# Optimization experiments

Hardware: AMD Instinct MI355X
Metric: run time of the kernel (lower is better)

The kernel has to match this reference:

```python
import jax, jax.numpy as jnp
import numpy as np

EPS = 1e-7


def setup_inputs() -> dict:
    key = jax.random.key(0)
    k1, k2, k3 = jax.random.split(key, 3)
    B, Nt, Nv, D = 64, 128, 256, 512
    text_feats = jax.random.normal(k1, (B, Nt, D), dtype=jnp.float32)
    visual_feats = jax.random.normal(k2, (B, Nv, D), dtype=jnp.float32)
    attention_mask = jax.random.randint(k3, (B, Nt), 0, 2, dtype=jnp.int32)
    return {"text_feats": text_feats, "visual_feats": visual_feats,
            "attention_mask": attention_mask}


def _l2norm(x):
    return x / jnp.clip(jnp.linalg.norm(x, axis=-1, keepdims=True), 1e-12)


def reference(text_feats, visual_feats, attention_mask):
    # Normalize token features (F.normalize along D)
    t = _l2norm(text_feats)            # (B, Nt, D)
    v = _l2norm(visual_feats)          # (B, Nv, D)
    # All-pairs token similarities: (B, B, Nt, Nv)
    token_sims = jnp.einsum('itd,jvd->ijtv', t, v)
    # Max over visual tokens -> (B, B, Nt)
    max_sims = jnp.max(token_sims, axis=3)
    # Masked mean over text tokens -> (B, B)
    mask = attention_mask.astype(jnp.float32)[:, None, :]   # (B, 1, Nt) broadcasts over pairs
    masked_sum = jnp.sum(max_sims * mask, axis=2)            # (B, B)
    valid = jnp.clip(jnp.sum(mask, axis=2), EPS)             # (B, 1)
    clip_sims = masked_sum / valid                           # (B, B)
    # Symmetric InfoNCE on the diagonal
    B = clip_sims.shape[0]
    diag = jnp.arange(B)
    losses_t2v = -jax.nn.log_softmax(clip_sims, axis=1)[diag, diag]
    losses_v2t = -jax.nn.log_softmax(clip_sims.T, axis=1)[diag, diag]
    contrastive_loss = jnp.mean(losses_t2v + losses_v2t) / 2.0
    # Regularization: keep negative token sims near zero
    neg_sims = jnp.clip(token_sims, -20.0, 0.0)
    reg_loss = 0.15 * jnp.mean(neg_sims ** 2)
    return contrastive_loss + reg_loss
```

## Files before the change

### kernel.cpp

```cpp
#include <hip/hip_runtime.h>
#include <hip/hip_bf16.h>

#define BB 64
#define NT 128
#define NV 256
#define DD 512
#define BKB 128
#define EPSF 1e-7f

typedef __attribute__((ext_vector_type(8))) int i32x8;
typedef __attribute__((ext_vector_type(4))) int i32x4;
typedef __attribute__((ext_vector_type(4))) float f32x4;

__device__ __forceinline__ void glds16(const uchar* g, uchar* l) {
    __builtin_amdgcn_global_load_lds(
        (const __attribute__((address_space(1))) unsigned int*)g,
        (__attribute__((address_space(3))) unsigned int*)l, 16, 0, 0);
}

__global__ __launch_bounds__(256) void k_normalize(
    const float* __restrict__ tf, const float* __restrict__ vf,
    uchar* __restrict__ tn, uchar* __restrict__ vn,
    float* __restrict__ reg_sum) {
    if (blockIdx.x == 0 && threadIdx.x == 0) *reg_sum = 0.0f;
    const int w = threadIdx.x >> 6, l = threadIdx.x & 63;
    const int row = blockIdx.x * 4 + w;
    const float* src;
    uchar* dst;
    if (row < BB * NT) {
        src = tf + (size_t)row * DD;
        dst = tn + (size_t)row * DD;
    } else {
        int r = row - BB * NT;
        src = vf + (size_t)r * DD;
        dst = vn + (size_t)r * DD;
    }
    float4 x0 = ((const float4*)src)[l * 2];
    float4 x1 = ((const float4*)src)[l * 2 + 1];
    float ss = x0.x * x0.x + x0.y * x0.y + x0.z * x0.z + x0.w * x0.w
             + x1.x * x1.x + x1.y * x1.y + x1.z * x1.z + x1.w * x1.w;
    #pragma unroll
    for (int off = 32; off; off >>= 1) ss += __shfl_xor(ss, off, 64);
    float scale = 1.0f / fmaxf(sqrtf(ss), 1e-12f);
    int p0 = __builtin_amdgcn_cvt_pk_fp8_f32(x0.x * scale, x0.y * scale, 0, 0);
    p0 = __builtin_amdgcn_cvt_pk_fp8_f32(x0.z * scale, x0.w * scale, p0, 1);
    int p1 = __builtin_amdgcn_cvt_pk_fp8_f32(x1.x * scale, x1.y * scale, 0, 0);
    p1 = __builtin_amdgcn_cvt_pk_fp8_f32(x1.z * scale, x1.w * scale, p1, 1);
    ((uint2*)dst)[l] = make_uint2((unsigned)p0, (unsigned)p1);
}

__global__ __launch_bounds__(512, 2) void k_gemm(
    const uchar* __restrict__ tn, const uchar* __restrict__ vn,
    const int* __restrict__ mask,
    float* __restrict__ clip_sims, float* __restrict__ reg_sum) {
    __shared__ uchar sT[NT * BKB];
    __shared__ uchar sV[NV * BKB];
    __shared__ float maxbuf[NT][4];
    __shared__ float redw[8];
    __shared__ float c0[2], c1[2];

    const int i = blockIdx.x, j = blockIdx.y;
    const int tid = threadIdx.x;
    const int l = tid & 63, w = tid >> 6;
    const int wr = w >> 2, wc = w & 3;
    const int m15 = l & 15, q = l >> 4;

    const uchar* tbase = tn + (size_t)i * NT * DD;
    const uchar* vbase = vn + (size_t)j * NV * DD;

    int t_off[2], v_off[4];
    #pragma unroll
    for (int s = 0; s < 2; ++s) {
        int f = s * 512 + tid;
        int r = f >> 3, p = f & 7, g = (p - r) & 7;
        t_off[s] = r * DD + g * 16;
    }
    #pragma unroll
    for (int s = 0; s < 4; ++s) {
        int f = s * 512 + tid;
        int r = f >> 3, p = f & 7, g = (p - r) & 7;
        v_off[s] = r * DD + g * 16;
    }

    int a_b0[4], a_b1[4], b_b0[4], b_b1[4];
    #pragma unroll
    for (int rt = 0; rt < 4; ++rt) {
        int row = wr * 64 + rt * 16 + m15;
        a_b0[rt] = row * BKB + (((2 * q + row) & 7) * 16);
        a_b1[rt] = row * BKB + (((2 * q + 1 + row) & 7) * 16);
    }
    #pragma unroll
    for (int ct = 0; ct < 4; ++ct) {
        int row = wc * 64 + ct * 16 + m15;
        b_b0[ct] = row * BKB + (((2 * q + row) & 7) * 16);
        b_b1[ct] = row * BKB + (((2 * q + 1 + row) & 7) * 16);
    }

    f32x4 acc[4][4];
    #pragma unroll
    for (int rt = 0; rt < 4; ++rt)
        #pragma unroll
        for (int ct = 0; ct < 4; ++ct) acc[rt][ct] = (f32x4){0.f, 0.f, 0.f, 0.f};

    for (int kk = 0; kk < DD; kk += BKB) {
        #pragma unroll
        for (int s = 0; s < 2; ++s)
            glds16(tbase + t_off[s] + kk, sT + (s * 512 + tid) * 16);
        #pragma unroll
        for (int s = 0; s < 4; ++s)
            glds16(vbase + v_off[s] + kk, sV + (s * 512 + tid) * 16);
        __syncthreads();

        i32x8 a[4];
        #pragma unroll
        for (int rt = 0; rt < 4; ++rt) {
            i32x4 lo = *(const i32x4*)(sT + a_b0[rt]);
            i32x4 hi = *(const i32x4*)(sT + a_b1[rt]);
            a[rt] = (i32x8){lo.x, lo.y, lo.z, lo.w, hi.x, hi.y, hi.z, hi.w};
        }
        #pragma unroll
        for (int ct = 0; ct < 4; ++ct) {
            i32x4 lo = *(const i32x4*)(sV + b_b0[ct]);
            i32x4 hi = *(const i32x4*)(sV + b_b1[ct]);
            i32x8 b = (i32x8){lo.x, lo.y, lo.z, lo.w, hi.x, hi.y, hi.z, hi.w};
            #pragma unroll
            for (int rt = 0; rt < 4; ++rt)
                acc[rt][ct] = __builtin_amdgcn_mfma_scale_f32_16x16x128_f8f6f4(
                    a[rt], b, acc[rt][ct],
                    0 , 0 ,
                    0, 127 , 0, 127 );
        }
        __syncthreads();
    }

    float rp = 0.0f;
    #pragma unroll
    for (int rt = 0; rt < 4; ++rt)
        #pragma unroll
        for (int ct = 0; ct < 4; ++ct)
            #pragma unroll
            for (int r = 0; r < 4; ++r) {
                float m = fminf(acc[rt][ct][r], 0.0f);
                rp = fmaf(m, m, rp);
            }

    #pragma unroll
    for (int rt = 0; rt < 4; ++rt)
        #pragma unroll
        for (int r = 0; r < 4; ++r) {
            float m = acc[rt][0][r];
            #pragma unroll
            for (int ct = 1; ct < 4; ++ct) m = fmaxf(m, acc[rt][ct][r]);
            #pragma unroll
            for (int msk = 1; msk < 16; msk <<= 1)
                m = fmaxf(m, __shfl_xor(m, msk, 64));
            if (m15 == 0)
                maxbuf[wr * 64 + rt * 16 + q * 4 + r][wc] = m;
        }

    #pragma unroll
    for (int off = 32; off; off >>= 1) rp += __shfl_down(rp, off, 64);
    if (l == 0) redw[w] = rp;
    __syncthreads();

    if (tid < NT) {
        float rm = fmaxf(fmaxf(maxbuf[tid][0], maxbuf[tid][1]),
                         fmaxf(maxbuf[tid][2], maxbuf[tid][3]));
        float mf = (float)mask[i * NT + tid];
        float v = rm * mf;
        #pragma unroll
        for (int off = 32; off; off >>= 1) {
            v += __shfl_down(v, off, 64);
            mf += __shfl_down(mf, off, 64);
        }
        if (l == 0) { c0[w] = v; c1[w] = mf; }
    }
    __syncthreads();
    if (tid == 0) {
        clip_sims[i * BB + j] = (c0[0] + c0[1]) / fmaxf(c1[0] + c1[1], EPSF);
        float s = 0.0f;
        #pragma unroll
        for (int x = 0; x < 8; ++x) s += redw[x];
        atomicAdd(reg_sum, s);
    }
}

__global__ __launch_bounds__(256) void k_loss(
    const float* __restrict__ clip_sims, const float* __restrict__ reg_sum,
    float* __restrict__ out) {
    __shared__ float sc[BB][BB + 1];
    __shared__ float lrow[BB], lcol[BB];
    int tid = threadIdx.x;
    for (int idx = tid; idx < BB * BB; idx += 256)
        sc[idx / BB][idx % BB] = clip_sims[idx];
    __syncthreads();
    if (tid < BB) {
        int i = tid;
        float m = sc[i][0];
        #pragma unroll
        for (int j = 1; j < BB; ++j) m = fmaxf(m, sc[i][j]);
        float s = 0.0f;
        #pragma unroll
        for (int j = 0; j < BB; ++j) s += expf(sc[i][j] - m);
        lrow[i] = m + logf(s) - sc[i][i];
    } else if (tid < 2 * BB) {
        int i = tid - BB;
        float m = sc[0][i];
        #pragma unroll
        for (int j = 1; j < BB; ++j) m = fmaxf(m, sc[j][i]);
        float s = 0.0f;
        #pragma unroll
        for (int j = 0; j < BB; ++j) s += expf(sc[j][i] - m);
        lcol[i] = m + logf(s) - sc[i][i];
    }
    __syncthreads();
    if (tid == 0) {
        float tot = 0.0f;
        for (int i = 0; i < BB; ++i) tot += lrow[i] + lcol[i];
        float contrastive = tot / (2.0f * BB);
        double denom = (double)BB * BB * NT * NV;
        float reg = 0.15f * (float)((double)reg_sum[0] / denom);
        out[0] = contrastive + reg;
    }
}

extern "C" void kernel_launch(void* const* d_in, const int* in_sizes, int n_in,
                              void* d_out, int out_size, void* d_ws, size_t ws_size,
                              hipStream_t stream) {
    const float* tf = (const float*)d_in[0];
    const float* vf = (const float*)d_in[1];
    const int* mask = (const int*)d_in[2];
    float* out = (float*)d_out;

    char* ws = (char*)d_ws;
    size_t tn_bytes = (size_t)BB * NT * DD;
    size_t vn_bytes = (size_t)BB * NV * DD;
    size_t cs_bytes = (size_t)BB * BB * sizeof(float);

    uchar* tn = (uchar*)ws;
    uchar* vn = (uchar*)(ws + tn_bytes);
    float* clip_sims = (float*)(ws + tn_bytes + vn_bytes);
    float* reg_sum = (float*)(ws + tn_bytes + vn_bytes + cs_bytes);

    k_normalize<<<(BB * NT + BB * NV) / 4, 256, 0, stream>>>(tf, vf, tn, vn, reg_sum);
    k_gemm<<<dim3(BB, BB), 512, 0, stream>>>(tn, vn, mask, clip_sims, reg_sum);
    k_loss<<<1, 256, 0, stream>>>(clip_sims, reg_sum, out);
}
```

Baseline: 250.0 us.

## Enlarge GEMM tile to two text samples, double-buffer LDS, swizzle block order

Each GEMM block now handles two text samples (256 rows) against one visual sample, so every B tile loaded into LDS is reused across twice as many rows. The K loop is fully unrolled and double-buffered, so the next K slice is prefetched into the alternate LDS buffer while MFMAs run on the current one. A 1D grid with a block-index swizzle groups blocks to improve L2 locality. In exchange the accumulators double to 128 floats per thread and LDS use grows to about 128KB, which may lower occupancy and cause register spills.

After: 419.5 us. +67.8%, slower.

```diff
diff --git a/kernel.cpp b/kernel.cpp
--- a/kernel.cpp
+++ b/kernel.cpp
@@ -6,6 +6,8 @@
 #define NV 256
 #define DD 512
 #define BKB 128
+#define BM 256
+#define BN 256
 #define EPSF 1e-7f
 
 typedef __attribute__((ext_vector_type(8))) int i32x8;
@@ -53,39 +55,37 @@
     const uchar* __restrict__ tn, const uchar* __restrict__ vn,
     const int* __restrict__ mask,
     float* __restrict__ clip_sims, float* __restrict__ reg_sum) {
-    __shared__ uchar sT[NT * BKB];
-    __shared__ uchar sV[NV * BKB];
-    __shared__ float maxbuf[NT][4];
+    __shared__ uchar sT[2][BM * BKB];
+    __shared__ uchar sV[2][BN * BKB];
+    __shared__ float maxbuf[BM][4];
     __shared__ float redw[8];
-    __shared__ float c0[2], c1[2];
-
-    const int i = blockIdx.x, j = blockIdx.y;
+    __shared__ float c0[4], c1[4];
+
+    const int bid = blockIdx.x;
+    const int swz = (bid & 7) * 256 + (bid >> 3);
+    const int bx = swz & 31;
+    const int by = swz >> 5;
+
     const int tid = threadIdx.x;
     const int l = tid & 63, w = tid >> 6;
     const int wr = w >> 2, wc = w & 3;
     const int m15 = l & 15, q = l >> 4;
 
-    const uchar* tbase = tn + (size_t)i * NT * DD;
-    const uchar* vbase = vn + (size_t)j * NV * DD;
-
-    int t_off[2], v_off[4];
-    #pragma unroll
-    for (int s = 0; s < 2; ++s) {
-        int f = s * 512 + tid;
-        int r = f >> 3, p = f & 7, g = (p - r) & 7;
-        t_off[s] = r * DD + g * 16;
-    }
+    const uchar* tbase = tn + (size_t)bx * BM * DD;
+    const uchar* vbase = vn + (size_t)by * NV * DD;
+
+    int soff[4];
     #pragma unroll
     for (int s = 0; s < 4; ++s) {
         int f = s * 512 + tid;
         int r = f >> 3, p = f & 7, g = (p - r) & 7;
-        v_off[s] = r * DD + g * 16;
-    }
-
-    int a_b0[4], a_b1[4], b_b0[4], b_b1[4];
-    #pragma unroll
-    for (int rt = 0; rt < 4; ++rt) {
-        int row = wr * 64 + rt * 16 + m15;
+        soff[s] = r * DD + g * 16;
+    }
+
+    int a_b0[8], a_b1[8], b_b0[4], b_b1[4];
+    #pragma unroll
+    for (int rt = 0; rt < 8; ++rt) {
+        int row = wr * 128 + rt * 16 + m15;
         a_b0[rt] = row * BKB + (((2 * q + row) & 7) * 16);
         a_b1[rt] = row * BKB + (((2 * q + 1 + row) & 7) * 16);
     }
@@ -96,46 +96,57 @@
         b_b1[ct] = row * BKB + (((2 * q + 1 + row) & 7) * 16);
     }
 
-    f32x4 acc[4][4];
-    #pragma unroll
-    for (int rt = 0; rt < 4; ++rt)
+    f32x4 acc[8][4];
+    #pragma unroll
+    for (int rt = 0; rt < 8; ++rt)
         #pragma unroll
         for (int ct = 0; ct < 4; ++ct) acc[rt][ct] = (f32x4){0.f, 0.f, 0.f, 0.f};
 
-    for (int kk = 0; kk < DD; kk += BKB) {
-        #pragma unroll
-        for (int s = 0; s < 2; ++s)
-            glds16(tbase + t_off[s] + kk, sT + (s * 512 + tid) * 16);
-        #pragma unroll
-        for (int s = 0; s < 4; ++s)
-            glds16(vbase + v_off[s] + kk, sV + (s * 512 + tid) * 16);
-        __syncthreads();
-
-        i32x8 a[4];
-        #pragma unroll
-        for (int rt = 0; rt < 4; ++rt) {
-            i32x4 lo = *(const i32x4*)(sT + a_b0[rt]);
-            i32x4 hi = *(const i32x4*)(sT + a_b1[rt]);
-            a[rt] = (i32x8){lo.x, lo.y, lo.z, lo.w, hi.x, hi.y, hi.z, hi.w};
-        }
+    #pragma unroll
+    for (int s = 0; s < 4; ++s) {
+        glds16(tbase + soff[s], sT[0] + (s * 512 + tid) * 16);
+        glds16(vbase + soff[s], sV[0] + (s * 512 + tid) * 16);
+    }
+    __syncthreads();
+
+    #pragma unroll
+    for (int ks = 0; ks < 4; ++ks) {
+        const int cur = ks & 1, nxt = cur ^ 1;
+        if (ks < 3) {
+            const int kk = (ks + 1) * BKB;
+            #pragma unroll
+            for (int s = 0; s < 4; ++s) {
+                glds16(tbase + soff[s] + kk, sT[nxt] + (s * 512 + tid) * 16);
+                glds16(vbase + soff[s] + kk, sV[nxt] + (s * 512 + tid) * 16);
+            }
+        }
+
+        i32x8 b[4];
         #pragma unroll
         for (int ct = 0; ct < 4; ++ct) {
-            i32x4 lo = *(const i32x4*)(sV + b_b0[ct]);
-            i32x4 hi = *(const i32x4*)(sV + b_b1[ct]);
-            i32x8 b = (i32x8){lo.x, lo.y, lo.z, lo.w, hi.x, hi.y, hi.z, hi.w};
-            #pragma unroll
-            for (int rt = 0; rt < 4; ++rt)
+            i32x4 lo = *(const i32x4*)(sV[cur] + b_b0[ct]);
+            i32x4 hi = *(const i32x4*)(sV[cur] + b_b1[ct]);
+            b[ct] = (i32x8){lo.x, lo.y, lo.z, lo.w, hi.x, hi.y, hi.z, hi.w};
+        }
+        #pragma unroll
+        for (int rt = 0; rt < 8; ++rt) {
+            i32x4 lo = *(const i32x4*)(sT[cur] + a_b0[rt]);
+            i32x4 hi = *(const i32x4*)(sT[cur] + a_b1[rt]);
+            i32x8 a = (i32x8){lo.x, lo.y, lo.z, lo.w, hi.x, hi.y, hi.z, hi.w};
+            #pragma unroll
+            for (int ct = 0; ct < 4; ++ct)
                 acc[rt][ct] = __builtin_amdgcn_mfma_scale_f32_16x16x128_f8f6f4(
-                    a[rt], b, acc[rt][ct],
+                    a, b[ct], acc[rt][ct],
                     0 , 0 ,
                     0, 127 , 0, 127 );
         }
+
         __syncthreads();
     }
 
     float rp = 0.0f;
     #pragma unroll
-    for (int rt = 0; rt < 4; ++rt)
+    for (int rt = 0; rt < 8; ++rt)
         #pragma unroll
         for (int ct = 0; ct < 4; ++ct)
             #pragma unroll
@@ -145,7 +156,7 @@
             }
 
     #pragma unroll
-    for (int rt = 0; rt < 4; ++rt)
+    for (int rt = 0; rt < 8; ++rt)
         #pragma unroll
         for (int r = 0; r < 4; ++r) {
             float m = acc[rt][0][r];
@@ -155,7 +166,7 @@
             for (int msk = 1; msk < 16; msk <<= 1)
                 m = fmaxf(m, __shfl_xor(m, msk, 64));
             if (m15 == 0)
-                maxbuf[wr * 64 + rt * 16 + q * 4 + r][wc] = m;
+                maxbuf[wr * 128 + rt * 16 + q * 4 + r][wc] = m;
         }
 
     #pragma unroll
@@ -163,10 +174,11 @@
     if (l == 0) redw[w] = rp;
     __syncthreads();
 
-    if (tid < NT) {
+    if (tid < 256) {
         float rm = fmaxf(fmaxf(maxbuf[tid][0], maxbuf[tid][1]),
                          fmaxf(maxbuf[tid][2], maxbuf[tid][3]));
-        float mf = (float)mask[i * NT + tid];
+        int ib = bx * 2 + (tid >> 7);
+        float mf = (float)mask[ib * NT + (tid & 127)];
         float v = rm * mf;
         #pragma unroll
         for (int off = 32; off; off >>= 1) {
@@ -177,7 +189,10 @@
     }
     __syncthreads();
     if (tid == 0) {
-        clip_sims[i * BB + j] = (c0[0] + c0[1]) / fmaxf(c1[0] + c1[1], EPSF);
+        clip_sims[(bx * 2) * BB + by] =
+            (c0[0] + c0[1]) / fmaxf(c1[0] + c1[1], EPSF);
+        clip_sims[(bx * 2 + 1) * BB + by] =
+            (c0[2] + c0[3]) / fmaxf(c1[2] + c1[3], EPSF);
         float s = 0.0f;
         #pragma unroll
         for (int x = 0; x < 8; ++x) s += redw[x];
@@ -243,6 +258,6 @@
     float* reg_sum = (float*)(ws + tn_bytes + vn_bytes + cs_bytes);
 
     k_normalize<<<(BB * NT + BB * NV) / 4, 256, 0, stream>>>(tf, vf, tn, vn, reg_sum);
-    k_gemm<<<dim3(BB, BB), 512, 0, stream>>>(tn, vn, mask, clip_sims, reg_sum);
+    k_gemm<<<32 * 64, 512, 0, stream>>>(tn, vn, mask, clip_sims, reg_sum);
     k_loss<<<1, 256, 0, stream>>>(clip_sims, reg_sum, out);
 }
```

## Double-buffer LDS tiles in fp8 GEMM to overlap loads with MFMA

Applied to the files above, without the earlier changes.

The K loop of the pairwise-similarity GEMM is unrolled into a two-buffer ping-pong. Each global-to-LDS prefetch of the next K slice is issued before the MFMA work on the current slice, and one barrier per stage replaces two. The aim is to hide global load latency behind compute within a single block. Shared memory per block doubles to about 96KB, which probably stops two blocks from fitting on a CU and so cuts the overlap that came from running blocks concurrently.

New measurement: 233.1 us. 6.8% less time.

```diff
diff --git a/kernel.cpp b/kernel.cpp
--- a/kernel.cpp
+++ b/kernel.cpp
@@ -53,8 +53,10 @@
     const uchar* __restrict__ tn, const uchar* __restrict__ vn,
     const int* __restrict__ mask,
     float* __restrict__ clip_sims, float* __restrict__ reg_sum) {
-    __shared__ uchar sT[NT * BKB];
-    __shared__ uchar sV[NV * BKB];
+    __shared__ uchar sT0[NT * BKB];
+    __shared__ uchar sT1[NT * BKB];
+    __shared__ uchar sV0[NV * BKB];
+    __shared__ uchar sV1[NV * BKB];
     __shared__ float maxbuf[NT][4];
     __shared__ float redw[8];
     __shared__ float c0[2], c1[2];
@@ -102,36 +104,52 @@
         #pragma unroll
         for (int ct = 0; ct < 4; ++ct) acc[rt][ct] = (f32x4){0.f, 0.f, 0.f, 0.f};
 
-    for (int kk = 0; kk < DD; kk += BKB) {
+    auto stage = [&](uchar* dT, uchar* dV, int kk) {
         #pragma unroll
         for (int s = 0; s < 2; ++s)
-            glds16(tbase + t_off[s] + kk, sT + (s * 512 + tid) * 16);
+            glds16(tbase + t_off[s] + kk, dT + (s * 512 + tid) * 16);
         #pragma unroll
         for (int s = 0; s < 4; ++s)
-            glds16(vbase + v_off[s] + kk, sV + (s * 512 + tid) * 16);
-        __syncthreads();
-
-        i32x8 a[4];
+            glds16(vbase + v_off[s] + kk, dV + (s * 512 + tid) * 16);
+    };
+    auto compute = [&](const uchar* bT, const uchar* bV) {
+        i32x8 bf[4];
+        #pragma unroll
+        for (int ct = 0; ct < 4; ++ct) {
+            i32x4 lo = *(const i32x4*)(bV + b_b0[ct]);
+            i32x4 hi = *(const i32x4*)(bV + b_b1[ct]);
+            bf[ct] = (i32x8){lo.x, lo.y, lo.z, lo.w, hi.x, hi.y, hi.z, hi.w};
+        }
         #pragma unroll
         for (int rt = 0; rt < 4; ++rt) {
-            i32x4 lo = *(const i32x4*)(sT + a_b0[rt]);
-            i32x4 hi = *(const i32x4*)(sT + a_b1[rt]);
-            a[rt] = (i32x8){lo.x, lo.y, lo.z, lo.w, hi.x, hi.y, hi.z, hi.w};
-        }
-        #pragma unroll
-        for (int ct = 0; ct < 4; ++ct) {
-            i32x4 lo = *(const i32x4*)(sV + b_b0[ct]);
-            i32x4 hi = *(const i32x4*)(sV + b_b1[ct]);
-            i32x8 b = (i32x8){lo.x, lo.y, lo.z, lo.w, hi.x, hi.y, hi.z, hi.w};
-            #pragma unroll
-            for (int rt = 0; rt < 4; ++rt)
+            i32x4 lo = *(const i32x4*)(bT + a_b0[rt]);
+            i32x4 hi = *(const i32x4*)(bT + a_b1[rt]);
+            i32x8 a = (i32x8){lo.x, lo.y, lo.z, lo.w, hi.x, hi.y, hi.z, hi.w};
+            #pragma unroll
+            for (int ct = 0; ct < 4; ++ct)
                 acc[rt][ct] = __builtin_amdgcn_mfma_scale_f32_16x16x128_f8f6f4(
-                    a[rt], b, acc[rt][ct],
+                    a, bf[ct], acc[rt][ct],
                     0 , 0 ,
                     0, 127 , 0, 127 );
         }
-        __syncthreads();
-    }
+    };
+
+    stage(sT0, sV0, 0);
+    __syncthreads();
+
+    stage(sT1, sV1, 1 * BKB);
+    compute(sT0, sV0);
+    __syncthreads();
+
+    stage(sT0, sV0, 2 * BKB);
+    compute(sT1, sV1);
+    __syncthreads();
+
+    stage(sT1, sV1, 3 * BKB);
+    compute(sT0, sV0);
+    __syncthreads();
+
+    compute(sT1, sV1);
 
     float rp = 0.0f;
     #pragma unroll
```
